# Performance work log

Hardware: AMD Instinct MI355X
Metric: run time of the kernel (lower is better)

Reference implementation:

```python
import jax, jax.numpy as jnp
import numpy as np

N_FEAT = 6
EMBED = 256
PAIRS = N_FEAT * (N_FEAT - 1) // 2  # 15
B, S = 32, 512


def setup_inputs() -> dict:
    key = jax.random.key(0)
    k1, k2, k3, k4, k5, k6 = jax.random.split(key, 6)
    features = jax.random.normal(k1, (N_FEAT, B, S, EMBED), dtype=jnp.float32)
    W_pair = jax.random.normal(k2, (PAIRS, 2 * EMBED, EMBED), dtype=jnp.float32) * 0.05
    b_pair = jax.random.normal(k3, (PAIRS, EMBED), dtype=jnp.float32) * 0.05
    W_final = jax.random.normal(k4, (PAIRS * EMBED, EMBED), dtype=jnp.float32) * 0.02
    b_final = jax.random.normal(k5, (EMBED,), dtype=jnp.float32) * 0.02
    NAS = jax.random.randint(k6, (N_FEAT,), 0, 2, dtype=jnp.int32)
    return {"features": features, "W_pair": W_pair, "b_pair": b_pair,
            "W_final": W_final, "b_final": b_final, "NAS": NAS}


def reference(features, W_pair, b_pair, W_final, b_final, NAS):
    n = features.shape[0]
    # static pair index order matches the nested loops: (0,1),(0,2),...,(n-2,n-1)
    i_idx, j_idx = np.triu_indices(n, k=1)
    nas = NAS.at[:2].set(1)  # encoder_input=True forces first two features on
    pair_mask = (nas[i_idx] * nas[j_idx]).astype(features.dtype)  # [P]
    # pairwise concat + linear + tanh, batched over all P pairs
    xcat = jnp.concatenate([features[i_idx], features[j_idx]], axis=-1)  # [P,B,S,2D]
    h = jnp.tanh(jnp.einsum('pbsk,pkd->pbsd', xcat, W_pair) + b_pair[:, None, None, :])
    h = h * pair_mask[:, None, None, None]  # zero out inactive pairs (ZeroNormal)
    P, Bb, Ss, D = h.shape
    # concat along last dim in pair order, then final linear
    flat = jnp.transpose(h, (1, 2, 0, 3)).reshape(Bb, Ss, P * D)  # [B,S,P*D]
    return flat @ W_final + b_final
```

## Files before the change

### kernel.cpp

```cpp
#include <hip/hip_runtime.h>
#include <hip/hip_bf16.h>


typedef unsigned short u16;
typedef __bf16 bf16x8 __attribute__((ext_vector_type(8)));
typedef float f32x4 __attribute__((ext_vector_type(4)));
typedef float f32x8 __attribute__((ext_vector_type(8)));

#define BS 16384
#define EMB 256
#define PAIRS 15

__constant__ int c_pi[PAIRS] = {0,0,0,0,0,1,1,1,1,2,2,2,3,3,4};
__constant__ int c_pj[PAIRS] = {1,2,3,4,5,2,3,4,5,3,4,5,4,5,5};

__device__ __forceinline__ u16 f2bf_u(float x) {
    __bf16 b = (__bf16)x;
    return __builtin_bit_cast(u16, b);
}

__global__ __launch_bounds__(256) void transpose_cvt(
    const float* __restrict__ in, u16* __restrict__ out, int R, int C)
{
    __shared__ float t[32][33];
    const int p  = blockIdx.z;
    const int r0 = blockIdx.x * 32;
    const int c0 = blockIdx.y * 32;
    const int tr = threadIdx.x >> 5;
    const int tc = threadIdx.x & 31;
    const float* ip = in + (size_t)p * R * C;
    u16* op = out + (size_t)p * C * R;
#pragma unroll
    for (int pass = 0; pass < 4; ++pass)
        t[pass * 8 + tr][tc] = ip[(size_t)(r0 + pass * 8 + tr) * C + c0 + tc];
    __syncthreads();
#pragma unroll
    for (int pass = 0; pass < 4; ++pass)
        op[(size_t)(c0 + pass * 8 + tr) * R + r0 + tc] =
            f2bf_u(t[tc][pass * 8 + tr]);
}


__device__ __forceinline__ void stage_tile(const u16* gsrc, int row_stride_us,
                                           int col_off_us, u16* lds_base, int tid) {
    int wave = tid >> 6;
#pragma unroll
    for (int r = 0; r < 2; ++r) {
        int c  = r * 512 + tid;
        int n  = c & 255;
        int kb = c >> 8;
        const u16* g = gsrc + (size_t)n * row_stride_us + col_off_us + kb * 8;
        u16* l = lds_base + (size_t)(r * 512 + wave * 64) * 8;
        __builtin_amdgcn_global_load_lds(
            (const __attribute__((address_space(1))) void*)g,
            (__attribute__((address_space(3))) void*)l,
            16, 0, 0);
    }
}

__global__ __launch_bounds__(512) void fused_cblock(
    const float* __restrict__ feats,
    const u16* __restrict__ Wp_t,
    const float* __restrict__ b_pair,
    const u16* __restrict__ Wf_t,
    const float* __restrict__ b_final,
    const int* __restrict__ NAS,
    float* __restrict__ out)
{
    __shared__ u16 lds_b[2][8192];
    __shared__ u16 lds_h[64 * 264];

    const int tid  = threadIdx.x;
    const int lane = tid & 63;
    const int wave = tid >> 6;
    const int wm   = wave & 3;
    const int wn   = wave >> 2;
    const int quad = lane >> 4;
    const int l16  = lane & 15;
    const int t0   = blockIdx.x * 64;

    const f32x4 fzero = {0.f, 0.f, 0.f, 0.f};
    f32x4 acc2[8];
#pragma unroll
    for (int i = 0; i < 8; ++i) acc2[i] = fzero;

    int nasv[6];
#pragma unroll
    for (int f = 0; f < 6; ++f) nasv[f] = (f < 2) ? 1 : (NAS[f] != 0 ? 1 : 0);

    const int arow = t0 + wm * 16 + l16;

    for (int p = 0; p < PAIRS; ++p) {
        const int fi = c_pi[p], fj = c_pj[p];
        if (!(nasv[fi] & nasv[fj])) continue;

        const u16* WpT = Wp_t + (size_t)p * 256 * 512;

        f32x4 acc1[8];
#pragma unroll
        for (int i = 0; i < 8; ++i) acc1[i] = fzero;

        stage_tile(WpT, 512, 0, lds_b[0], tid);
        __syncthreads();
        for (int ks = 0; ks < 16; ++ks) {
            const int cur = ks & 1;
            if (ks < 15) stage_tile(WpT, 512, (ks + 1) * 32, lds_b[1 - cur], tid);
            const float* fsrc = feats + (size_t)((ks < 8) ? fi : fj) * BS * EMB;
            f32x8 af = *(const f32x8*)(fsrc + (size_t)arow * EMB +
                                       ((ks & 7) * 32) + quad * 8);
            bf16x8 a;
#pragma unroll
            for (int i = 0; i < 8; ++i) a[i] = (__bf16)af[i];
#pragma unroll
            for (int nt = 0; nt < 8; ++nt) {
                const int n = wn * 128 + nt * 16 + l16;
                bf16x8 b = *(const bf16x8*)(&lds_b[cur][(quad * 256 + n) * 8]);
                acc1[nt] = __builtin_amdgcn_mfma_f32_16x16x32_bf16(a, b, acc1[nt], 0, 0, 0);
            }
            __syncthreads();
        }

#pragma unroll
        for (int nt = 0; nt < 8; ++nt) {
            const int n = wn * 128 + nt * 16 + l16;
            const float bias = b_pair[p * 256 + n];
#pragma unroll
            for (int r = 0; r < 4; ++r) {
                const int row = wm * 16 + quad * 4 + r;
                lds_h[row * 264 + n] = f2bf_u(tanhf(acc1[nt][r] + bias));
            }
        }

        stage_tile(Wf_t, 3840, p * 256, lds_b[0], tid);
        __syncthreads();
        for (int ks = 0; ks < 8; ++ks) {
            const int cur = ks & 1;
            if (ks < 7) stage_tile(Wf_t, 3840, p * 256 + (ks + 1) * 32, lds_b[1 - cur], tid);
            const int e0 = ks * 32 + quad * 8;
            const int row = wm * 16 + l16;
            bf16x8 a = *(const bf16x8*)(&lds_h[row * 264 + e0]);
#pragma unroll
            for (int nt = 0; nt < 8; ++nt) {
                const int n = wn * 128 + nt * 16 + l16;
                bf16x8 b = *(const bf16x8*)(&lds_b[cur][(quad * 256 + n) * 8]);
                acc2[nt] = __builtin_amdgcn_mfma_f32_16x16x32_bf16(a, b, acc2[nt], 0, 0, 0);
            }
            __syncthreads();
        }
    }

#pragma unroll
    for (int nt = 0; nt < 8; ++nt) {
        const int n = wn * 128 + nt * 16 + l16;
        const float bf = b_final[n];
#pragma unroll
        for (int r = 0; r < 4; ++r) {
            const int t = t0 + wm * 16 + quad * 4 + r;
            out[(size_t)t * EMB + n] = acc2[nt][r] + bf;
        }
    }
}


#define TOK 4

__global__ __launch_bounds__(256) void fallback_cblock(
    const float* __restrict__ feats, const float* __restrict__ W_pair,
    const float* __restrict__ b_pair, const float* __restrict__ W_final,
    const float* __restrict__ b_final, const int* __restrict__ NAS,
    float* __restrict__ out)
{
    __shared__ float xs[TOK][6 * 256];
    __shared__ float hf[TOK][PAIRS * 256];

    const int n  = threadIdx.x;
    const int t0 = blockIdx.x * TOK;

#pragma unroll
    for (int tk = 0; tk < TOK; ++tk)
#pragma unroll
        for (int f = 0; f < 6; ++f)
            xs[tk][f * 256 + n] = feats[((size_t)f * BS + t0 + tk) * EMB + n];
    __syncthreads();

    int nasv[6];
#pragma unroll
    for (int f = 0; f < 6; ++f) nasv[f] = (f < 2) ? 1 : (NAS[f] != 0 ? 1 : 0);

    for (int p = 0; p < PAIRS; ++p) {
        const int fi = c_pi[p], fj = c_pj[p];
        if (!(nasv[fi] & nasv[fj])) {
#pragma unroll
            for (int tk = 0; tk < TOK; ++tk) hf[tk][p * 256 + n] = 0.f;
            continue;
        }
        float acc[TOK];
        const float bias = b_pair[p * 256 + n];
#pragma unroll
        for (int tk = 0; tk < TOK; ++tk) acc[tk] = bias;
        const float* Wp = W_pair + (size_t)p * 512 * 256;
#pragma unroll 4
        for (int k = 0; k < 512; ++k) {
            const float w = Wp[(size_t)k * 256 + n];
            const int xoff = ((k < 256) ? fi : fj) * 256 + (k & 255);
#pragma unroll
            for (int tk = 0; tk < TOK; ++tk) acc[tk] += xs[tk][xoff] * w;
        }
#pragma unroll
        for (int tk = 0; tk < TOK; ++tk)
            hf[tk][p * 256 + n] = tanhf(acc[tk]);
    }
    __syncthreads();

    float acc[TOK];
    const float bf = b_final[n];
#pragma unroll
    for (int tk = 0; tk < TOK; ++tk) acc[tk] = bf;
#pragma unroll 4
    for (int k = 0; k < PAIRS * 256; ++k) {
        const float w = W_final[(size_t)k * 256 + n];
#pragma unroll
        for (int tk = 0; tk < TOK; ++tk) acc[tk] += hf[tk][k] * w;
    }
#pragma unroll
    for (int tk = 0; tk < TOK; ++tk)
        out[(size_t)(t0 + tk) * EMB + n] = acc[tk];
}


extern "C" void kernel_launch(void* const* d_in, const int* in_sizes, int n_in,
                              void* d_out, int out_size, void* d_ws, size_t ws_size,
                              hipStream_t stream) {
    const float* feats   = (const float*)d_in[0];
    const float* W_pair  = (const float*)d_in[1];
    const float* b_pair  = (const float*)d_in[2];
    const float* W_final = (const float*)d_in[3];
    const float* b_final = (const float*)d_in[4];
    const int*   NAS     = (const int*)d_in[5];

    const size_t needed = ((size_t)PAIRS * 256 * 512 + (size_t)256 * 3840) * 2;

    if (ws_size >= needed) {
        u16* Wp_t = (u16*)d_ws;
        u16* Wf_t = Wp_t + (size_t)PAIRS * 256 * 512;
        transpose_cvt<<<dim3(512 / 32, 256 / 32, PAIRS), 256, 0, stream>>>(
            W_pair, Wp_t, 512, 256);
        transpose_cvt<<<dim3(3840 / 32, 256 / 32, 1), 256, 0, stream>>>(
            W_final, Wf_t, 3840, 256);
        fused_cblock<<<BS / 64, 512, 0, stream>>>(feats, Wp_t, b_pair, Wf_t,
                                                  b_final, NAS, (float*)d_out);
    } else {
        fallback_cblock<<<BS / TOK, 256, 0, stream>>>(feats, W_pair, b_pair,
                                                      W_final, b_final, NAS,
                                                      (float*)d_out);
    }
}
```

Measured before the change: 182.2 us.

## Prefetch next stage weight tiles across GEMM phases and merge transpose launches

In the fused kernel, the first weight tile of the next GEMM phase now loads during the last k-step of the current phase. W_final's first tile is fetched during the last W_pair step, and the next active pair's first W_pair tile during the last W_final step. This removes the exposed load-and-sync bubble at each phase boundary. The active-pair mask is computed once as a bitmask, the two weight transpose kernels are merged into one launch (at the cost of many blocks that exit early), and launch_bounds gains a min-blocks hint of 4, which may tighten register allocation and risk spills.

```diff
diff --git a/kernel.cpp b/kernel.cpp
--- a/kernel.cpp
+++ b/kernel.cpp
@@ -19,25 +19,29 @@
     return __builtin_bit_cast(u16, b);
 }
 
-__global__ __launch_bounds__(256) void transpose_cvt(
-    const float* __restrict__ in, u16* __restrict__ out, int R, int C)
+__global__ __launch_bounds__(256) void transpose_cvt2(
+    const float* __restrict__ Wp, const float* __restrict__ Wf,
+    u16* __restrict__ Wp_t, u16* __restrict__ Wf_t)
 {
     __shared__ float t[32][33];
-    const int p  = blockIdx.z;
+    const int z = blockIdx.z;
+    const float* in;
+    u16* out;
+    int R;
+    if (z < PAIRS) { R = 512;  in = Wp + (size_t)z * 512 * 256; out = Wp_t + (size_t)z * 256 * 512; }
+    else           { R = 3840; in = Wf;                          out = Wf_t; }
     const int r0 = blockIdx.x * 32;
+    if (r0 >= R) return;
     const int c0 = blockIdx.y * 32;
     const int tr = threadIdx.x >> 5;
     const int tc = threadIdx.x & 31;
-    const float* ip = in + (size_t)p * R * C;
-    u16* op = out + (size_t)p * C * R;
 #pragma unroll
     for (int pass = 0; pass < 4; ++pass)
-        t[pass * 8 + tr][tc] = ip[(size_t)(r0 + pass * 8 + tr) * C + c0 + tc];
+        t[pass * 8 + tr][tc] = in[(size_t)(r0 + pass * 8 + tr) * 256 + c0 + tc];
     __syncthreads();
 #pragma unroll
     for (int pass = 0; pass < 4; ++pass)
-        op[(size_t)(c0 + pass * 8 + tr) * R + r0 + tc] =
-            f2bf_u(t[tc][pass * 8 + tr]);
+        out[(size_t)(c0 + pass * 8 + tr) * R + r0 + tc] = f2bf_u(t[tc][pass * 8 + tr]);
 }
 
 
@@ -58,7 +62,7 @@
     }
 }
 
-__global__ __launch_bounds__(512) void fused_cblock(
+__global__ __launch_bounds__(512, 4) void fused_cblock(
     const float* __restrict__ feats,
     const u16* __restrict__ Wp_t,
     const float* __restrict__ b_pair,
@@ -79,6 +83,8 @@
     const int l16  = lane & 15;
     const int t0   = blockIdx.x * 64;
 
+    stage_tile(Wp_t, 512, 0, lds_b[0], tid);
+
     const f32x4 fzero = {0.f, 0.f, 0.f, 0.f};
     f32x4 acc2[8];
 #pragma unroll
@@ -87,24 +93,30 @@
     int nasv[6];
 #pragma unroll
     for (int f = 0; f < 6; ++f) nasv[f] = (f < 2) ? 1 : (NAS[f] != 0 ? 1 : 0);
+    int pmask = 0;
+#pragma unroll
+    for (int p = 0; p < PAIRS; ++p)
+        if (nasv[c_pi[p]] & nasv[c_pj[p]]) pmask |= (1 << p);
 
     const int arow = t0 + wm * 16 + l16;
 
+    __syncthreads();
+
     for (int p = 0; p < PAIRS; ++p) {
+        if (!((pmask >> p) & 1)) continue;
         const int fi = c_pi[p], fj = c_pj[p];
-        if (!(nasv[fi] & nasv[fj])) continue;
-
         const u16* WpT = Wp_t + (size_t)p * 256 * 512;
+        const int rest  = pmask >> (p + 1);
+        const int pnext = rest ? (p + 1 + __builtin_ctz(rest)) : -1;
 
         f32x4 acc1[8];
 #pragma unroll
         for (int i = 0; i < 8; ++i) acc1[i] = fzero;
 
-        stage_tile(WpT, 512, 0, lds_b[0], tid);
-        __syncthreads();
         for (int ks = 0; ks < 16; ++ks) {
             const int cur = ks & 1;
             if (ks < 15) stage_tile(WpT, 512, (ks + 1) * 32, lds_b[1 - cur], tid);
+            else         stage_tile(Wf_t, 3840, p * 256, lds_b[1 - cur], tid);
             const float* fsrc = feats + (size_t)((ks < 8) ? fi : fj) * BS * EMB;
             f32x8 af = *(const f32x8*)(fsrc + (size_t)arow * EMB +
                                        ((ks & 7) * 32) + quad * 8);
@@ -130,12 +142,14 @@
                 lds_h[row * 264 + n] = f2bf_u(tanhf(acc1[nt][r] + bias));
             }
         }
-
-        stage_tile(Wf_t, 3840, p * 256, lds_b[0], tid);
         __syncthreads();
+
         for (int ks = 0; ks < 8; ++ks) {
             const int cur = ks & 1;
-            if (ks < 7) stage_tile(Wf_t, 3840, p * 256 + (ks + 1) * 32, lds_b[1 - cur], tid);
+            if (ks < 7)
+                stage_tile(Wf_t, 3840, p * 256 + (ks + 1) * 32, lds_b[1 - cur], tid);
+            else if (pnext >= 0)
+                stage_tile(Wp_t + (size_t)pnext * 256 * 512, 512, 0, lds_b[1 - cur], tid);
             const int e0 = ks * 32 + quad * 8;
             const int row = wm * 16 + l16;
             bf16x8 a = *(const bf16x8*)(&lds_h[row * 264 + e0]);
@@ -243,10 +257,8 @@
     if (ws_size >= needed) {
         u16* Wp_t = (u16*)d_ws;
         u16* Wf_t = Wp_t + (size_t)PAIRS * 256 * 512;
-        transpose_cvt<<<dim3(512 / 32, 256 / 32, PAIRS), 256, 0, stream>>>(
-            W_pair, Wp_t, 512, 256);
-        transpose_cvt<<<dim3(3840 / 32, 256 / 32, 1), 256, 0, stream>>>(
-            W_final, Wf_t, 3840, 256);
+        transpose_cvt2<<<dim3(3840 / 32, 256 / 32, PAIRS + 1), 256, 0, stream>>>(
+            W_pair, W_final, Wp_t, Wf_t);
         fused_cblock<<<BS / 64, 512, 0, stream>>>(feats, Wp_t, b_pair, Wf_t,
                                                   b_final, NAS, (float*)d_out);
     } else {
```

New measurement: 183.6 us. Within noise of the previous version (+0.8%).
